# Kernel tuning notes

Measured on AMD Instinct MI355X. Metric: run time of the kernel, lower is better.

## Reference

```python
import jax, jax.numpy as jnp
import numpy as np

C, H, R, INTER = 1024, 16, 16, 2816  # hidden, heads, lora rank, mlp intermediate
B, N = 2, 2048
EPS = 1e-5


def setup_inputs() -> dict:
    key = jax.random.key(0)
    ks = iter(jax.random.split(key, 48))
    w = lambda shape: jax.random.normal(next(ks), shape, jnp.float32) * 0.02
    d = {}
    d["x"] = jax.random.normal(next(ks), (B, N, C), jnp.float32)
    d["y"] = jax.random.normal(next(ks), (B, N, C), jnp.float32)
    d["c"] = jax.random.normal(next(ks), (B, C), jnp.float32)
    # LayerNorms
    d["gx_w"] = jnp.ones((C,)); d["gx_b"] = jnp.zeros((C,))
    d["gy_w"] = jnp.ones((C,)); d["gy_b"] = jnp.zeros((C,))
    # adaLN: SiLU -> Linear(C, 6C)
    d["ada_w"] = w((C, 6 * C)); d["ada_b"] = jnp.zeros((6 * C,))
    # two DoRA cross-attentions
    for p in ("xy", "yx"):
        d[p + "_qkv"] = w((C, 3 * C))
        d[p + "_mag"] = jnp.ones((1, H, 1, 1))
        d[p + "_la"] = w((C, R))
        d[p + "_lb"] = w((R, C))
        d[p + "_proj"] = w((C, C))
    # two HGRN recurrent attentions
    for p in ("ax", "ay"):
        d[p + "_wi"] = w((C, C))
        d[p + "_wf"] = w((C, C))
        d[p + "_wg"] = w((C, C))
        d[p + "_wo"] = w((C, C))
        d[p + "_gn"] = jnp.ones((C,))
    # two gated MLPs
    for p in ("mx", "my"):
        d[p + "_gate"] = w((C, 2 * INTER))
        d[p + "_down"] = w((INTER, C))
    return d


def _ln(v, wgt, b):
    m = v.mean(-1, keepdims=True)
    var = ((v - m) ** 2).mean(-1, keepdims=True)
    return (v - m) / jnp.sqrt(var + EPS) * wgt + b


def _modulate(v, shift, scale):
    return v * (1.0 + scale[:, None, :]) + shift[:, None, :]


def _dora_attn(q_in, Wqkv, mag, la, lb, Wp):
    # NOTE: source ignores key/value args -> self-attention on query stream
    Bq, Nq, Cq = q_in.shape
    D = Cq // H
    qkv = (q_in @ Wqkv).reshape(Bq, Nq, 3, H, D).transpose(2, 0, 3, 1, 4)
    q, k, v = qkv[0], qkv[1], qkv[2]  # [B,H,N,D]
    delta = (q_in @ la) @ lb  # LoRA delta injected into Q
    q = q + mag * delta.reshape(Bq, Nq, H, D).transpose(0, 2, 1, 3)
    attn = jax.nn.softmax(jnp.einsum('bhnd,bhmd->bhnm', q, k) * (D ** -0.5), axis=-1)
    o = jnp.einsum('bhnm,bhmd->bhnd', attn, v).transpose(0, 2, 1, 3).reshape(Bq, Nq, Cq)
    return o @ Wp


def _hgrn_attn(v, wi, wf, wg, wo, gn):
    Bv, Nv, Cv = v.shape
    D = Cv // H
    f = jax.nn.sigmoid(v @ wf)
    i = jax.nn.silu(v @ wi) * (1.0 - f)
    def step(h, ft_it):
        ft, it = ft_it
        h = ft * h + it
        return h, h
    _, hs = jax.lax.scan(step, jnp.zeros((Bv, Cv), v.dtype),
                         (f.transpose(1, 0, 2), i.transpose(1, 0, 2)))
    h = hs.transpose(1, 0, 2).reshape(Bv, Nv, H, D)
    h = h / jnp.sqrt((h * h).mean(-1, keepdims=True) + EPS)  # per-head RMSNorm
    h = (h * gn.reshape(H, D)).reshape(Bv, Nv, Cv)
    return (h * jax.nn.silu(v @ wg)) @ wo


def _mlp(v, wgate, wdown):
    u = v @ wgate
    gate, val = jnp.split(u, 2, axis=-1)
    return (jax.nn.silu(gate) * val) @ wdown


def reference(x, y, c, gx_w, gx_b, gy_w, gy_b, ada_w, ada_b,
              xy_qkv, xy_mag, xy_la, xy_lb, xy_proj,
              yx_qkv, yx_mag, yx_la, yx_lb, yx_proj,
              ax_wi, ax_wf, ax_wg, ax_wo, ax_gn,
              ay_wi, ay_wf, ay_wg, ay_wo, ay_gn,
              mx_gate, mx_down, my_gate, my_down):
    mods = jax.nn.silu(c) @ ada_w + ada_b
    sh_msa, sc_msa, g_msa, sh_mlp, sc_mlp, g_mlp = jnp.split(mods, 6, axis=1)
    x_norm = _ln(x, gx_w, gx_b)
    y_norm = _ln(y, gy_w, gy_b)
    x = x + g_msa[:, None, :] * _dora_attn(x_norm, xy_qkv, xy_mag, xy_la, xy_lb, xy_proj)
    y = y + g_msa[:, None, :] * _dora_attn(y_norm, yx_qkv, yx_mag, yx_la, yx_lb, yx_proj)
    x = x + g_msa[:, None, :] * _hgrn_attn(_modulate(x_norm, sh_msa, sc_msa), ax_wi, ax_wf, ax_wg, ax_wo, ax_gn)
    y = y + g_msa[:, None, :] * _hgrn_attn(_modulate(y_norm, sh_msa, sc_msa), ay_wi, ay_wf, ay_wg, ay_wo, ay_gn)
    x = x + g_mlp[:, None, :] * _mlp(_modulate(_ln(x, gx_w, gx_b), sh_mlp, sc_mlp), mx_gate, mx_down)
    y = y + g_mlp[:, None, :] * _mlp(_modulate(_ln(y, gy_w, gy_b), sh_mlp, sc_mlp), my_gate, my_down)
    return (x, y)
```

## Files before the change

kernel.cpp:

```cpp
#include <hip/hip_runtime.h>
#include <stdint.h>

#define NTOK 2048
#define CDIM 1024
#define ROWS 4096
#define MODS_STRIDE 6144
#define INTERDIM 2816
#define NCHUNK 32
#define CHLEN (NTOK/NCHUNK)

typedef unsigned short u16;
typedef __bf16 bf16x8 __attribute__((ext_vector_type(8)));
typedef float f32x4 __attribute__((ext_vector_type(4)));
typedef float f32x16 __attribute__((ext_vector_type(16)));
typedef u16 u16x8 __attribute__((ext_vector_type(8)));
typedef unsigned int u32x4 __attribute__((ext_vector_type(4)));

__device__ __forceinline__ float b2f(u16 u){
  union { unsigned int i; float f; } v; v.i = ((unsigned int)u) << 16; return v.f;
}
__device__ __forceinline__ u16 f2b(float f){
  union { float f; unsigned int i; } v; v.f = f;
  unsigned int i = v.i;
  unsigned int r = i + 0x7FFFu + ((i >> 16) & 1u);
  return (u16)(r >> 16);
}
__device__ __forceinline__ float sigm(float x){ return 1.f/(1.f+__expf(-x)); }
__device__ __forceinline__ float wredsum(float v){
#pragma unroll
  for (int o=32;o>0;o>>=1) v += __shfl_xor(v,o);
  return v;
}
__device__ __forceinline__ void async16(const void* g, void* l){
  __builtin_amdgcn_global_load_lds(
      (const __attribute__((address_space(1))) unsigned int*)g,
      (__attribute__((address_space(3))) unsigned int*)l, 16, 0, 0);
}
__device__ __forceinline__ unsigned cvt_pk_bf16(float lo, float hi){
  unsigned r;
  asm("v_cvt_pk_bf16_f32 %0, %1, %2" : "=v"(r) : "v"(lo), "v"(hi));
  return r;
}
__device__ __forceinline__ void permlane32_swap(unsigned &a, unsigned &b){
  asm volatile("v_permlane32_swap_b32 %0, %1" : "+v"(a), "+v"(b));
}

__global__ __launch_bounds__(512) void gemm_bt(
    const u16* __restrict__ Ain, const u16* __restrict__ Bt,
    int M, int N, int K, int epi,
    u16* __restrict__ outB,
    float* __restrict__ dest, const float* __restrict__ gate)
{
  __shared__ u16 smem[2][2][2][8192];

  const int nwg  = gridDim.x * gridDim.y;
  const int orig = blockIdx.y * gridDim.x + blockIdx.x;
  const int qch  = nwg >> 3, rch = nwg & 7;
  const int xcd  = orig & 7, loc = orig >> 3;
  const int swzb = (xcd < rch ? xcd*(qch+1) : rch*(qch+1) + (xcd-rch)*qch) + loc;
  const int m0 = (swzb / gridDim.x) * 256;
  const int n0 = (swzb % gridDim.x) * 256;

  const int kchunk = K / gridDim.z;
  const int kbase  = blockIdx.z * kchunk;
  const int NT = kchunk >> 6;

  const int tid = threadIdx.x;
  const int w = tid >> 6, lane = tid & 63;
  const int quad = lane >> 4, l16 = lane & 15;
  const int wm = w >> 2, wn = w & 3;
  const int sx = (l16 & 7) << 4;

  int soff[2];
#pragma unroll
  for (int j=0;j<2;++j){
    const int row = (w*2 + j)*8 + (lane >> 3);
    soff[j] = row*(K*2) + (((lane & 7) ^ (row & 7)) << 4);
  }

  const char* pA0 = (const char*)(Ain + (size_t)m0*K       + kbase);
  const char* pA1 = (const char*)(Ain + (size_t)(m0+128)*K + kbase);
  const char* pB0 = (const char*)(Bt  + (size_t)n0*K       + kbase);
  const char* pB1 = (const char*)(Bt  + (size_t)(n0+128)*K + kbase);

  auto stage = [&](const char* base, int t, u16* region){
#pragma unroll
    for (int j=0;j<2;++j)
      async16(base + (size_t)t*128 + soff[j], (char*)region + (w*2+j)*1024);
  };

  f32x4 acc[8][4] = {};
  bf16x8 af[4][2];
  bf16x8 bq[4][2];

  stage(pA0, 0, &smem[0][0][0][0]);
  stage(pA1, 0, &smem[0][0][1][0]);
  stage(pB0, 0, &smem[0][1][0][0]);
  stage(pB1, 0, &smem[0][1][1][0]);
  if (NT > 1){
    stage(pA0, 1, &smem[1][0][0][0]);
    asm volatile("s_waitcnt vmcnt(2)" ::: "memory");
  } else {
    asm volatile("s_waitcnt vmcnt(0)" ::: "memory");
  }
  __builtin_amdgcn_s_barrier();

#pragma unroll 1
  for (int t=0; t<NT; ++t){
    const int s  = t & 1;
    const int s1 = s ^ 1;
    const char* Ah = (const char*)&smem[s][0][wm][0];
    const char* Bh = (const char*)&smem[s][1][wn>>1][0];
    const int bb = (wn & 1) * 64;

#pragma unroll
    for (int mf=0; mf<4; ++mf)
#pragma unroll
      for (int ks=0; ks<2; ++ks){
        const int b = ((mf*16 + l16)*128 + ks*64 + quad*16) ^ sx;
        af[mf][ks] = *reinterpret_cast<const bf16x8*>(Ah + b);
      }
#pragma unroll
    for (int nf=0; nf<2; ++nf)
#pragma unroll
      for (int ks=0; ks<2; ++ks){
        const int b = ((bb + nf*16 + l16)*128 + ks*64 + quad*16) ^ sx;
        bq[nf][ks] = *reinterpret_cast<const bf16x8*>(Bh + b);
      }
    if (t+1 < NT) stage(pA1, t+1, &smem[s1][0][1][0]);
    __builtin_amdgcn_sched_barrier(0);
    __builtin_amdgcn_s_barrier();
    asm volatile("s_waitcnt lgkmcnt(0)" ::: "memory");
    __builtin_amdgcn_sched_barrier(0);
    __builtin_amdgcn_s_setprio(1);
#pragma unroll
    for (int mf=0; mf<4; ++mf)
#pragma unroll
      for (int nf=0; nf<2; ++nf)
#pragma unroll
        for (int ks=0; ks<2; ++ks)
          acc[mf][nf] = __builtin_amdgcn_mfma_f32_16x16x32_bf16(af[mf][ks], bq[nf][ks], acc[mf][nf], 0,0,0);
    __builtin_amdgcn_s_setprio(0);
    __builtin_amdgcn_sched_barrier(0);
    __builtin_amdgcn_s_barrier();

#pragma unroll
    for (int nf=0; nf<2; ++nf)
#pragma unroll
      for (int ks=0; ks<2; ++ks){
        const int b = ((bb + (2+nf)*16 + l16)*128 + ks*64 + quad*16) ^ sx;
        bq[2+nf][ks] = *reinterpret_cast<const bf16x8*>(Bh + b);
      }
    if (t+1 < NT) stage(pB0, t+1, &smem[s1][1][0][0]);
    __builtin_amdgcn_sched_barrier(0);
    __builtin_amdgcn_s_barrier();
    asm volatile("s_waitcnt lgkmcnt(0)" ::: "memory");
    __builtin_amdgcn_sched_barrier(0);
    __builtin_amdgcn_s_setprio(1);
#pragma unroll
    for (int mf=0; mf<4; ++mf)
#pragma unroll
      for (int nf=0; nf<2; ++nf)
#pragma unroll
        for (int ks=0; ks<2; ++ks)
          acc[mf][2+nf] = __builtin_amdgcn_mfma_f32_16x16x32_bf16(af[mf][ks], bq[2+nf][ks], acc[mf][2+nf], 0,0,0);
    __builtin_amdgcn_s_setprio(0);
    __builtin_amdgcn_sched_barrier(0);
    __builtin_amdgcn_s_barrier();

#pragma unroll
    for (int mf=0; mf<4; ++mf)
#pragma unroll
      for (int ks=0; ks<2; ++ks){
        const int b = ((64 + mf*16 + l16)*128 + ks*64 + quad*16) ^ sx;
        af[mf][ks] = *reinterpret_cast<const bf16x8*>(Ah + b);
      }
    if (t+1 < NT) stage(pB1, t+1, &smem[s1][1][1][0]);
    __builtin_amdgcn_sched_barrier(0);
    __builtin_amdgcn_s_barrier();
    asm volatile("s_waitcnt lgkmcnt(0)" ::: "memory");
    __builtin_amdgcn_sched_barrier(0);
    __builtin_amdgcn_s_setprio(1);
#pragma unroll
    for (int mf=0; mf<4; ++mf)
#pragma unroll
      for (int nf=0; nf<2; ++nf)
#pragma unroll
        for (int ks=0; ks<2; ++ks)
          acc[4+mf][2+nf] = __builtin_amdgcn_mfma_f32_16x16x32_bf16(af[mf][ks], bq[2+nf][ks], acc[4+mf][2+nf], 0,0,0);
    __builtin_amdgcn_s_setprio(0);
    __builtin_amdgcn_sched_barrier(0);
    __builtin_amdgcn_s_barrier();

    if (t+2 < NT) stage(pA0, t+2, &smem[s][0][0][0]);
    __builtin_amdgcn_sched_barrier(0);
    __builtin_amdgcn_s_barrier();
    __builtin_amdgcn_s_setprio(1);
#pragma unroll
    for (int mf=0; mf<4; ++mf)
#pragma unroll
      for (int nf=0; nf<2; ++nf)
#pragma unroll
        for (int ks=0; ks<2; ++ks)
          acc[4+mf][nf] = __builtin_amdgcn_mfma_f32_16x16x32_bf16(af[mf][ks], bq[nf][ks], acc[4+mf][nf], 0,0,0);
    __builtin_amdgcn_s_setprio(0);
    __builtin_amdgcn_sched_barrier(0);
    if (t+2 < NT) asm volatile("s_waitcnt vmcnt(2)" ::: "memory");
    else          asm volatile("s_waitcnt vmcnt(0)" ::: "memory");
    __builtin_amdgcn_s_barrier();
  }

#pragma unroll
  for (int i=0;i<8;++i){
    const int row = m0 + wm*128 + (i>>2)*64 + (i&3)*16 + quad*4;
#pragma unroll
    for (int j=0;j<4;++j){
      const int col = n0 + wn*64 + j*16 + l16;
#pragma unroll
      for (int r=0;r<4;++r){
        const float v = acc[i][j][r];
        const size_t idx = (size_t)(row + r)*N + col;
        if (epi==1){ outB[idx] = f2b(v); }
        else {
          const int b = (row + r) >> 11;
          atomicAdd(&dest[idx], gate[b*MODS_STRIDE + col] * v);
        }
      }
    }
  }
}

struct TDesc { const float* src; u16* dst; int rows; int cols; int base; int dstride; int doff; };
struct TPack { TDesc d[16]; };

__global__ __launch_bounds__(256) void transpose_all(TPack p, int nmat)
{
  __shared__ float t[64][65];
  const int bid = blockIdx.x;
  int mi = 0;
#pragma unroll 1
  while (mi+1 < nmat && bid >= p.d[mi+1].base) ++mi;
  const TDesc D = p.d[mi];
  const int tid2   = bid - D.base;
  const int tilesx = D.cols >> 6;
  const int r0 = (tid2 / tilesx) * 64;
  const int c0 = (tid2 % tilesx) * 64;
  const int tx = threadIdx.x & 63, ty = threadIdx.x >> 6;
  for (int i=ty;i<64;i+=4)
    t[i][tx] = D.src[(size_t)(r0+i)*D.cols + c0 + tx];
  __syncthreads();
  const int wx = threadIdx.x & 31, wy = threadIdx.x >> 5;
  for (int c=wy;c<64;c+=8){
    const unsigned lo = f2b(t[2*wx  ][c]);
    const unsigned hi = f2b(t[2*wx+1][c]);
    *reinterpret_cast<unsigned*>(&D.dst[(size_t)(c0+c)*D.dstride + D.doff + r0 + 2*wx]) = lo | (hi<<16);
  }
}

__global__ __launch_bounds__(256) void lora_fold(
    const float* __restrict__ la, const float* __restrict__ lb,
    const float* __restrict__ mag, u16* __restrict__ WqkvT)
{
  const unsigned idx = blockIdx.x*256u + threadIdx.x;
  const int k = idx & 1023, n = idx >> 10;
  float s = 0.f;
#pragma unroll
  for (int r=0;r<16;++r)
    s = fmaf(la[k*16+r], lb[r*1024+n], s);
  const float m = mag[n>>6];
  const unsigned o = (unsigned)n*1024u + k;
  WqkvT[o] = f2b(b2f(WqkvT[o]) + m*s);
}

__global__ __launch_bounds__(256) void ln_kernel(
    const float* __restrict__ xin,
    const float* __restrict__ w, const float* __restrict__ bias,
    const float* __restrict__ mods, int sh_off, int sc_off,
    u16* __restrict__ out_norm, u16* __restrict__ out_mod,
    float* __restrict__ out_xw)
{
  const int row = blockIdx.x;
  const int b = row >> 11;
  const int t = threadIdx.x;
  float v[4];
#pragma unroll
  for (int e=0;e<4;++e)
    v[e] = xin[(size_t)row*CDIM + t*4+e];
  float s  = v[0]+v[1]+v[2]+v[3];
  float ss = v[0]*v[0]+v[1]*v[1]+v[2]*v[2]+v[3]*v[3];
  s = wredsum(s); ss = wredsum(ss);
  __shared__ float rs[4], rss[4];
  const int wv = t>>6;
  if ((t&63)==0){ rs[wv]=s; rss[wv]=ss; }
  __syncthreads();
  s  = rs[0]+rs[1]+rs[2]+rs[3];
  ss = rss[0]+rss[1]+rss[2]+rss[3];
  const float mean = s * (1.f/1024.f);
  const float var  = ss * (1.f/1024.f) - mean*mean;
  const float rinv = rsqrtf(var + 1e-5f);
#pragma unroll
  for (int e=0;e<4;++e){
    const int c = t*4+e;
    const float nv = (v[e]-mean)*rinv*w[c] + bias[c];
    if (out_norm) out_norm[(size_t)row*CDIM+c] = f2b(nv);
    if (out_mod){
      const float sc = mods[b*MODS_STRIDE + sc_off + c];
      const float sh = mods[b*MODS_STRIDE + sh_off + c];
      out_mod[(size_t)row*CDIM+c] = f2b(nv*(1.f+sc)+sh);
    }
    if (out_xw) out_xw[(size_t)row*CDIM+c] = v[e];
  }
}

__global__ __launch_bounds__(256) void ada_init(
    const float* __restrict__ ab, float* __restrict__ mods)
{
  const int j = blockIdx.x*256 + threadIdx.x;
  const int jj = (j >= MODS_STRIDE) ? j - MODS_STRIDE : j;
  mods[j] = ab[jj];
}

__global__ __launch_bounds__(256) void ada_split(
    const float* __restrict__ cin, const float* __restrict__ aw,
    float* __restrict__ mods)
{
  const int j  = blockIdx.x*256 + threadIdx.x;
  const int k0 = blockIdx.y*64;
  float s0 = 0.f, s1 = 0.f;
  for (int k=k0; k<k0+64; ++k){
    const float wv = aw[(size_t)k*MODS_STRIDE + j];
    const float c0 = cin[k], c1 = cin[CDIM + k];
    s0 = fmaf(c0*sigm(c0), wv, s0);
    s1 = fmaf(c1*sigm(c1), wv, s1);
  }
  atomicAdd(&mods[j], s0);
  atomicAdd(&mods[MODS_STRIDE + j], s1);
}

__global__ __launch_bounds__(256) void attn_mfma(
    const u16* __restrict__ qkv, u16* __restrict__ AH)
{
  __shared__ u16 Kl[64*64];
  __shared__ u16 Vt[64*64];
  const int t = threadIdx.x;
  const int w = t>>6, lane = t&63;
  const int l32 = lane & 31, hi = lane >> 5;
  const int qt = blockIdx.x, h = blockIdx.y, b = blockIdx.z;
  const size_t rowbase = (size_t)b*NTOK;

  bf16x8 qf[4];
  {
    const size_t gr = rowbase + qt*128 + w*32 + l32;
    const u16* qp = qkv + gr*3072 + h*64;
#pragma unroll
    for (int ds=0; ds<4; ++ds){
      const u16x8 qa = *reinterpret_cast<const u16x8*>(qp + ds*16 + hi*8);
#pragma unroll
      for (int j=0;j<8;++j)
        qf[ds][j] = (__bf16)(b2f(qa[j]) * 0.125f);
    }
  }

  const u16* ksrc[2]; int kwr[2];
#pragma unroll
  for (int it=0; it<2; ++it){
    const int e = it*256 + t;
    const int key = e>>3, ch = e&7;
    ksrc[it] = qkv + (rowbase + key)*3072 + 1024 + h*64 + ch*8;
    kwr[it]  = key*128 + ((ch ^ (key&7)) << 4);
  }
  const u16* vsrc[2]; int vwr[2][8];
#pragma unroll
  for (int it=0; it<2; ++it){
    const int d0 = (w*2 + it)*8;
    vsrc[it] = qkv + (rowbase + lane)*3072 + 2048 + h*64 + d0;
#pragma unroll
    for (int j=0;j<8;++j){
      const int d = d0 + j;
      vwr[it][j] = d*128 + (((lane>>3) ^ (d&7)) << 4) + (lane&7)*2;
    }
  }
  int kra[2][4];
#pragma unroll
  for (int st=0; st<2; ++st)
#pragma unroll
    for (int ds=0; ds<4; ++ds){
      const int key = st*32 + l32;
      kra[st][ds] = key*128 + (((ds*2 + hi) ^ (key&7)) << 4);
    }
  int vra[2][2][2];
#pragma unroll
  for (int st=0; st<2; ++st)
#pragma unroll
    for (int ks=0; ks<2; ++ks)
#pragma unroll
      for (int dt=0; dt<2; ++dt){
        const int d = dt*32 + l32;
        vra[st][ks][dt] = d*128 + (((st*4 + ks*2 + hi) ^ (d&7)) << 4);
      }

  const size_t KSTRIDE = (size_t)64*3072;

  u16x8 kA[2], vA[2], kB[2], vB[2];
#pragma unroll
  for (int it=0; it<2; ++it){
    kA[it] = *reinterpret_cast<const u16x8*>(ksrc[it]);
    vA[it] = *reinterpret_cast<const u16x8*>(vsrc[it]);
  }

  float l_part = 0.f;
  f32x16 oacc[2] = {};

  auto step = [&](u16x8 (&kk)[2], u16x8 (&vv)[2], int kbn,
                  u16x8 (&kn)[2], u16x8 (&vn)[2]){
#pragma unroll
    for (int it=0; it<2; ++it){
      *reinterpret_cast<u16x8*>((char*)Kl + kwr[it]) = kk[it];
#pragma unroll
      for (int j=0;j<8;++j)
        *reinterpret_cast<u16*>((char*)Vt + vwr[it][j]) = vv[it][j];
    }
    __syncthreads();
    {
      const size_t off = (size_t)kbn * KSTRIDE;
#pragma unroll
      for (int it=0; it<2; ++it){
        kn[it] = *reinterpret_cast<const u16x8*>(ksrc[it] + off);
        vn[it] = *reinterpret_cast<const u16x8*>(vsrc[it] + off);
      }
    }
    f32x16 sacc[2] = {};
#pragma unroll
    for (int st=0; st<2; ++st)
#pragma unroll
      for (int ds=0; ds<4; ++ds){
        const bf16x8 af = *reinterpret_cast<const bf16x8*>((char*)Kl + kra[st][ds]);
        sacc[st] = __builtin_amdgcn_mfma_f32_32x32x16_bf16(af, qf[ds], sacc[st], 0,0,0);
      }
#pragma unroll
    for (int st=0; st<2; ++st)
#pragma unroll
      for (int r=0;r<16;++r){
        const float pv = __expf(sacc[st][r]);
        sacc[st][r] = pv;
        l_part += pv;
      }
#pragma unroll
    for (int st=0; st<2; ++st){
      unsigned wd[8];
#pragma unroll
      for (int m=0;m<8;++m)
        wd[m] = cvt_pk_bf16(sacc[st][2*m], sacc[st][2*m+1]);
      permlane32_swap(wd[0], wd[2]);
      permlane32_swap(wd[1], wd[3]);
      permlane32_swap(wd[4], wd[6]);
      permlane32_swap(wd[5], wd[7]);
      u32x4 paw[2];
      paw[0] = u32x4{wd[0], wd[1], wd[2], wd[3]};
      paw[1] = u32x4{wd[4], wd[5], wd[6], wd[7]};
#pragma unroll
      for (int ks=0; ks<2; ++ks){
        const bf16x8 pa = *reinterpret_cast<const bf16x8*>(&paw[ks]);
#pragma unroll
        for (int dt=0; dt<2; ++dt){
          const bf16x8 vb = *reinterpret_cast<const bf16x8*>((char*)Vt + vra[st][ks][dt]);
          oacc[dt] = __builtin_amdgcn_mfma_f32_32x32x16_bf16(pa, vb, oacc[dt], 0,0,0);
        }
      }
    }
    __syncthreads();
  };

#pragma unroll 1
  for (int kb=0; kb<32; kb+=2){
    step(kA, vA, (kb+1 < 32 ? kb+1 : 31), kB, vB);
    step(kB, vB, (kb+2 < 32 ? kb+2 : 31), kA, vA);
  }

  const float l_run = l_part + __shfl_xor(l_part, 32);

#pragma unroll
  for (int r=0;r<16;++r){
    const int crow = (r&3) + 8*(r>>2) + 4*hi;
    const float li = __shfl(l_run, crow);
    const size_t grow = rowbase + qt*128 + w*32 + crow;
#pragma unroll
    for (int dt=0; dt<2; ++dt)
      AH[grow*2048 + h*64 + dt*32 + l32] = f2b(oacc[dt][r] / li);
  }
}

__global__ __launch_bounds__(256) void scan_p1(
    const u16* __restrict__ FIG, float* __restrict__ cA, float* __restrict__ cH)
{
  const unsigned int idx = blockIdx.x*256u + threadIdx.x;
  const unsigned int c = idx & 1023u, chunk = (idx>>10)&(NCHUNK-1), b = idx>>15;
  float A = 1.f, h = 0.f;
  const size_t base = ((size_t)b*NTOK + chunk*CHLEN) * 3072;
  for (int t=0;t<CHLEN;++t){
    const float F = b2f(FIG[base + (size_t)t*3072 + c]);
    const float I = b2f(FIG[base + (size_t)t*3072 + 1024 + c]);
    const float f = sigm(F);
    const float il = I*sigm(I) * (1.f - f);
    A *= f;
    h = fmaf(f, h, il);
  }
  cA[idx] = A; cH[idx] = h;
}

__global__ __launch_bounds__(256) void scan_p2(
    const float* __restrict__ cA, const float* __restrict__ cH, float* __restrict__ Hinit)
{
  const unsigned int idx = blockIdx.x*256u + threadIdx.x;
  const unsigned int b = idx>>10, c = idx&1023u;
  float h = 0.f;
#pragma unroll
  for (int ch=0;ch<NCHUNK;++ch){
    const unsigned int q = (b*NCHUNK + ch)*1024 + c;
    Hinit[q] = h;
    h = fmaf(cA[q], h, cH[q]);
  }
}

__global__ __launch_bounds__(256) void scan_p3(
    const u16* __restrict__ FIG, const float* __restrict__ Hinit, u16* __restrict__ Hb)
{
  const unsigned int idx = blockIdx.x*256u + threadIdx.x;
  const unsigned int c = idx & 1023u, chunk = (idx>>10)&(NCHUNK-1), b = idx>>15;
  float h = Hinit[idx];
  const size_t base = ((size_t)b*NTOK + chunk*CHLEN) * 3072;
  const size_t obase = ((size_t)b*NTOK + chunk*CHLEN) * CDIM;
  for (int t=0;t<CHLEN;++t){
    const float F = b2f(FIG[base + (size_t)t*3072 + c]);
    const float I = b2f(FIG[base + (size_t)t*3072 + 1024 + c]);
    const float f = sigm(F);
    const float il = I*sigm(I) * (1.f - f);
    h = fmaf(f, h, il);
    Hb[obase + (size_t)t*CDIM + c] = f2b(h);
  }
}

__global__ __launch_bounds__(256) void hgrn_post(
    const u16* __restrict__ Hb, const u16* __restrict__ FIG,
    const float* __restrict__ gn, u16* __restrict__ AH)
{
  const int row = blockIdx.x;
  const int t = threadIdx.x;
  float hv[4]; float ss = 0.f;
#pragma unroll
  for (int e=0;e<4;++e){
    hv[e] = b2f(Hb[(size_t)row*CDIM + t*4 + e]);
    ss = fmaf(hv[e], hv[e], ss);
  }
#pragma unroll
  for (int o=1;o<16;o<<=1) ss += __shfl_xor(ss, o);
  const float rinv = rsqrtf(ss*(1.f/64.f) + 1e-5f);
#pragma unroll
  for (int e=0;e<4;++e){
    const int c = t*4+e;
    const float g = b2f(FIG[(size_t)row*3072 + 2048 + c]);
    AH[(size_t)row*2048 + 1024 + c] = f2b(hv[e]*rinv*gn[c] * g*sigm(g));
  }
}

__global__ __launch_bounds__(256) void act_kernel(
    const u16* __restrict__ U, u16* __restrict__ A)
{
  const unsigned int i = blockIdx.x*256u + threadIdx.x;
  const unsigned int r = i / INTERDIM, j = i % INTERDIM;
  const float g = b2f(U[(size_t)r*(2*INTERDIM) + j]);
  const float v = b2f(U[(size_t)r*(2*INTERDIM) + INTERDIM + j]);
  A[i] = f2b(g*sigm(g)*v);
}

__global__ __launch_bounds__(256) void fill_fail(float* __restrict__ out)
{
  const unsigned int i = blockIdx.x*256u + threadIdx.x;
  out[i] = 1234.5f;
}

static void run_stream(hipStream_t stream,
    const float* Xin, const float* LNW, const float* LNB,
    const float* MAG, const float* LA, const float* LBw, const float* GN,
    float* mods, float* xw,
    u16* WqkvT, const u16* WpwT, const u16* WhgrnT,
    const u16* WgateT, const u16* WdownT,
    u16* x_norm, u16* v_h, u16* qkvb, u16* delta, u16* AH,
    float* cA, float* cH, float* Hinit, u16* U, u16* actb)
{
  u16* FIG    = qkvb;
  u16* Hb     = delta;
  u16* mlp_in = x_norm;

  lora_fold<<<4096,256,0,stream>>>(LA, LBw, MAG, WqkvT);

  ln_kernel<<<ROWS,256,0,stream>>>(Xin, LNW, LNB, mods, 0, 1024, x_norm, v_h, xw);

  gemm_bt<<<dim3(12,16),512,0,stream>>>(x_norm, WqkvT, ROWS,3072,1024, 1, qkvb, nullptr, nullptr);
  attn_mfma<<<dim3(16,16,2),256,0,stream>>>(qkvb, AH);

  gemm_bt<<<dim3(12,16),512,0,stream>>>(v_h, WhgrnT, ROWS,3072,1024, 1, FIG, nullptr, nullptr);
  scan_p1<<<2*NCHUNK*1024/256,256,0,stream>>>(FIG, cA, cH);
  scan_p2<<<8,256,0,stream>>>(cA, cH, Hinit);
  scan_p3<<<2*NCHUNK*1024/256,256,0,stream>>>(FIG, Hinit, Hb);
  hgrn_post<<<ROWS,256,0,stream>>>(Hb, FIG, GN, AH);

  gemm_bt<<<dim3(4,16,4),512,0,stream>>>(AH, WpwT, ROWS,1024,2048, 2, nullptr, xw, mods+2048);

  ln_kernel<<<ROWS,256,0,stream>>>(xw, LNW, LNB, mods, 3072, 4096, nullptr, mlp_in, nullptr);
  gemm_bt<<<dim3(22,16),512,0,stream>>>(mlp_in, WgateT, ROWS,5632,1024, 1, U, nullptr, nullptr);
  act_kernel<<<ROWS*INTERDIM/256,256,0,stream>>>(U, actb);
  gemm_bt<<<dim3(4,16,4),512,0,stream>>>(actb, WdownT, ROWS,1024,2816, 2, nullptr, xw, mods+5120);
}

extern "C" void kernel_launch(void* const* d_in, const int* in_sizes, int n_in,
                              void* d_out, int out_size, void* d_ws, size_t ws_size,
                              hipStream_t stream)
{
  const float* X    = (const float*)d_in[0];
  const float* Y    = (const float*)d_in[1];
  const float* Cc   = (const float*)d_in[2];
  const float* GXW  = (const float*)d_in[3];
  const float* GXB  = (const float*)d_in[4];
  const float* GYW  = (const float*)d_in[5];
  const float* GYB  = (const float*)d_in[6];
  const float* ADAW = (const float*)d_in[7];
  const float* ADAB = (const float*)d_in[8];
  const float* XY_QKV = (const float*)d_in[9];
  const float* XY_MAG = (const float*)d_in[10];
  const float* XY_LA  = (const float*)d_in[11];
  const float* XY_LB  = (const float*)d_in[12];
  const float* XY_PROJ= (const float*)d_in[13];
  const float* YX_QKV = (const float*)d_in[14];
  const float* YX_MAG = (const float*)d_in[15];
  const float* YX_LA  = (const float*)d_in[16];
  const float* YX_LB  = (const float*)d_in[17];
  const float* YX_PROJ= (const float*)d_in[18];
  const float* AX_WI = (const float*)d_in[19];
  const float* AX_WF = (const float*)d_in[20];
  const float* AX_WG = (const float*)d_in[21];
  const float* AX_WO = (const float*)d_in[22];
  const float* AX_GN = (const float*)d_in[23];
  const float* AY_WI = (const float*)d_in[24];
  const float* AY_WF = (const float*)d_in[25];
  const float* AY_WG = (const float*)d_in[26];
  const float* AY_WO = (const float*)d_in[27];
  const float* AY_GN = (const float*)d_in[28];
  const float* MX_GATE = (const float*)d_in[29];
  const float* MX_DOWN = (const float*)d_in[30];
  const float* MY_GATE = (const float*)d_in[31];
  const float* MY_DOWN = (const float*)d_in[32];
  float* OUT = (float*)d_out;

  char* p = (char*)d_ws;
  size_t off = 0;
  auto alloc = [&](size_t bytes)->char*{
    char* r = p + off;
    off = (off + bytes + 255) & ~(size_t)255;
    return r;
  };
  float* mods  = (float*)alloc(2*MODS_STRIDE*sizeof(float));
  u16* WqkvT0  = (u16*)alloc((size_t)3072*1024*2);
  u16* WqkvT1  = (u16*)alloc((size_t)3072*1024*2);
  u16* WpwT0   = (u16*)alloc((size_t)1024*2048*2);
  u16* WpwT1   = (u16*)alloc((size_t)1024*2048*2);
  u16* WhgrnT0 = (u16*)alloc((size_t)3072*1024*2);
  u16* WhgrnT1 = (u16*)alloc((size_t)3072*1024*2);
  u16* WgateT0 = (u16*)alloc((size_t)5632*1024*2);
  u16* WgateT1 = (u16*)alloc((size_t)5632*1024*2);
  u16* WdownT0 = (u16*)alloc((size_t)1024*2816*2);
  u16* WdownT1 = (u16*)alloc((size_t)1024*2816*2);
  u16* x_norm  = (u16*)alloc((size_t)ROWS*CDIM*2);
  u16* v_h     = (u16*)alloc((size_t)ROWS*CDIM*2);
  u16* qkvb    = (u16*)alloc((size_t)ROWS*3072*2);
  u16* delta   = (u16*)alloc((size_t)ROWS*CDIM*2);
  u16* AH      = (u16*)alloc((size_t)ROWS*2048*2);
  float* cA    = (float*)alloc((size_t)2*NCHUNK*1024*sizeof(float));
  float* cH    = (float*)alloc((size_t)2*NCHUNK*1024*sizeof(float));
  float* Hinit = (float*)alloc((size_t)2*NCHUNK*1024*sizeof(float));
  u16* U       = (u16*)alloc((size_t)ROWS*5632*2);
  u16* actb    = (u16*)alloc((size_t)ROWS*INTERDIM*2);

  if (off > ws_size){
    fill_fail<<<(2*ROWS*CDIM)/256,256,0,stream>>>(OUT);
    return;
  }

  ada_init<<<2*MODS_STRIDE/256,256,0,stream>>>(ADAB, mods);
  ada_split<<<dim3(MODS_STRIDE/256,16),256,0,stream>>>(Cc, ADAW, mods);

  TPack tp; int base = 0; int ndesc = 0;
  auto add = [&](const float* s, u16* d2, int rows, int cols, int dstride, int doff){
    tp.d[ndesc].src = s; tp.d[ndesc].dst = d2;
    tp.d[ndesc].rows = rows; tp.d[ndesc].cols = cols; tp.d[ndesc].base = base;
    tp.d[ndesc].dstride = dstride; tp.d[ndesc].doff = doff;
    base += (rows>>6)*(cols>>6); ++ndesc;
  };
  add(XY_QKV,  WqkvT0, 1024, 3072, 1024, 0);
  add(XY_PROJ, WpwT0,  1024, 1024, 2048, 0);
  add(AX_WO,   WpwT0,  1024, 1024, 2048, 1024);
  add(AX_WF, WhgrnT0,               1024, 1024, 1024, 0);
  add(AX_WI, WhgrnT0 + 1024*1024,   1024, 1024, 1024, 0);
  add(AX_WG, WhgrnT0 + 2*1024*1024, 1024, 1024, 1024, 0);
  add(MX_GATE, WgateT0, 1024, 5632, 1024, 0);
  add(MX_DOWN, WdownT0, 2816, 1024, 2816, 0);
  add(YX_QKV,  WqkvT1, 1024, 3072, 1024, 0);
  add(YX_PROJ, WpwT1,  1024, 1024, 2048, 0);
  add(AY_WO,   WpwT1,  1024, 1024, 2048, 1024);
  add(AY_WF, WhgrnT1,               1024, 1024, 1024, 0);
  add(AY_WI, WhgrnT1 + 1024*1024,   1024, 1024, 1024, 0);
  add(AY_WG, WhgrnT1 + 2*1024*1024, 1024, 1024, 1024, 0);
  add(MY_GATE, WgateT1, 1024, 5632, 1024, 0);
  add(MY_DOWN, WdownT1, 2816, 1024, 2816, 0);
  transpose_all<<<base,256,0,stream>>>(tp, ndesc);

  run_stream(stream, X, GXW, GXB, XY_MAG, XY_LA, XY_LB, AX_GN,
             mods, OUT,
             WqkvT0, WpwT0, WhgrnT0, WgateT0, WdownT0,
             x_norm, v_h, qkvb, delta, AH,
             cA, cH, Hinit, U, actb);

  run_stream(stream, Y, GYW, GYB, YX_MAG, YX_LA, YX_LB, AY_GN,
             mods, OUT + (size_t)ROWS*CDIM,
             WqkvT1, WpwT1, WhgrnT1, WgateT1, WdownT1,
             x_norm, v_h, qkvb, delta, AH,
             cA, cH, Hinit, U, actb);
}
```

Measured before the change: 1.175 ms.

## Batch the x and y streams into single launches per stage

Every stage kernel (lora_fold, LN, GEMMs, attention, scan, hgrn_post, act) now takes pointer pairs and picks its stream from the block index. Each stage runs for both streams in one launch with twice the grid, which halves the launch count and fills the GPU better on the smaller grids such as the split-K GEMMs and the scans. The cost is a separate workspace for each stream, roughly doubling intermediate memory. A sequential per-stream fallback is kept for when the workspace is too small.

```diff
diff --git a/kernel.cpp b/kernel.cpp
--- a/kernel.cpp
+++ b/kernel.cpp
@@ -46,12 +46,21 @@
 }
 
 __global__ __launch_bounds__(512) void gemm_bt(
-    const u16* __restrict__ Ain, const u16* __restrict__ Bt,
-    int M, int N, int K, int epi,
-    u16* __restrict__ outB,
-    float* __restrict__ dest, const float* __restrict__ gate)
+    const u16* __restrict__ A0, const u16* __restrict__ A1,
+    const u16* __restrict__ B0, const u16* __restrict__ B1,
+    int M, int N, int K, int zsplit, int epi,
+    u16* __restrict__ o0, u16* __restrict__ o1,
+    float* __restrict__ d0, float* __restrict__ d1,
+    const float* __restrict__ gate)
 {
   __shared__ u16 smem[2][2][2][8192];
+
+  const int zs = blockIdx.z / zsplit;
+  const int kz = blockIdx.z % zsplit;
+  const u16* Ain = zs ? A1 : A0;
+  const u16* Bt  = zs ? B1 : B0;
+  u16* outB  = zs ? o1 : o0;
+  float* dest = zs ? d1 : d0;
 
   const int nwg  = gridDim.x * gridDim.y;
   const int orig = blockIdx.y * gridDim.x + blockIdx.x;
@@ -61,8 +70,8 @@
   const int m0 = (swzb / gridDim.x) * 256;
   const int n0 = (swzb % gridDim.x) * 256;
 
-  const int kchunk = K / gridDim.z;
-  const int kbase  = blockIdx.z * kchunk;
+  const int kchunk = K / zsplit;
+  const int kbase  = kz * kchunk;
   const int NT = kchunk >> 6;
 
   const int tid = threadIdx.x;
@@ -258,29 +267,47 @@
 }
 
 __global__ __launch_bounds__(256) void lora_fold(
-    const float* __restrict__ la, const float* __restrict__ lb,
-    const float* __restrict__ mag, u16* __restrict__ WqkvT)
-{
-  const unsigned idx = blockIdx.x*256u + threadIdx.x;
+    const float* __restrict__ la0, const float* __restrict__ la1,
+    const float* __restrict__ lb0, const float* __restrict__ lb1,
+    const float* __restrict__ mg0, const float* __restrict__ mg1,
+    u16* __restrict__ W0, u16* __restrict__ W1)
+{
+  const unsigned g = blockIdx.x*256u + threadIdx.x;
+  const int s = g >> 20;
+  const unsigned idx = g & 1048575u;
+  const float* la = s ? la1 : la0;
+  const float* lb = s ? lb1 : lb0;
+  const float* mag = s ? mg1 : mg0;
+  u16* W = s ? W1 : W0;
   const int k = idx & 1023, n = idx >> 10;
-  float s = 0.f;
+  float sum = 0.f;
 #pragma unroll
   for (int r=0;r<16;++r)
-    s = fmaf(la[k*16+r], lb[r*1024+n], s);
+    sum = fmaf(la[k*16+r], lb[r*1024+n], sum);
   const float m = mag[n>>6];
   const unsigned o = (unsigned)n*1024u + k;
-  WqkvT[o] = f2b(b2f(WqkvT[o]) + m*s);
+  W[o] = f2b(b2f(W[o]) + m*sum);
 }
 
 __global__ __launch_bounds__(256) void ln_kernel(
-    const float* __restrict__ xin,
-    const float* __restrict__ w, const float* __restrict__ bias,
+    const float* __restrict__ x0, const float* __restrict__ x1,
+    const float* __restrict__ w0, const float* __restrict__ w1,
+    const float* __restrict__ bi0, const float* __restrict__ bi1,
     const float* __restrict__ mods, int sh_off, int sc_off,
-    u16* __restrict__ out_norm, u16* __restrict__ out_mod,
-    float* __restrict__ out_xw)
-{
-  const int row = blockIdx.x;
+    u16* __restrict__ on0, u16* __restrict__ on1,
+    u16* __restrict__ om0, u16* __restrict__ om1,
+    float* __restrict__ ox0, float* __restrict__ ox1)
+{
+  const int gr = blockIdx.x;
+  const int sid = gr >> 12;
+  const int row = gr & (ROWS-1);
   const int b = row >> 11;
+  const float* xin  = sid ? x1  : x0;
+  const float* w    = sid ? w1  : w0;
+  const float* bias = sid ? bi1 : bi0;
+  u16* out_norm = sid ? on1 : on0;
+  u16* out_mod  = sid ? om1 : om0;
+  float* out_xw = sid ? ox1 : ox0;
   const int t = threadIdx.x;
   float v[4];
 #pragma unroll
@@ -338,14 +365,19 @@
 }
 
 __global__ __launch_bounds__(256) void attn_mfma(
-    const u16* __restrict__ qkv, u16* __restrict__ AH)
+    const u16* __restrict__ q0, const u16* __restrict__ q1,
+    u16* __restrict__ A0, u16* __restrict__ A1)
 {
   __shared__ u16 Kl[64*64];
   __shared__ u16 Vt[64*64];
   const int t = threadIdx.x;
   const int w = t>>6, lane = t&63;
   const int l32 = lane & 31, hi = lane >> 5;
-  const int qt = blockIdx.x, h = blockIdx.y, b = blockIdx.z;
+  const int qt = blockIdx.x, h = blockIdx.y;
+  const int zb = blockIdx.z;
+  const int b = zb & 1, sid = zb >> 1;
+  const u16* qkv = sid ? q1 : q0;
+  u16* AH = sid ? A1 : A0;
   const size_t rowbase = (size_t)b*NTOK;
 
   bf16x8 qf[4];
@@ -491,10 +523,14 @@
 }
 
 __global__ __launch_bounds__(256) void scan_p1(
-    const u16* __restrict__ FIG, float* __restrict__ cA, float* __restrict__ cH)
-{
-  const unsigned int idx = blockIdx.x*256u + threadIdx.x;
-  const unsigned int c = idx & 1023u, chunk = (idx>>10)&(NCHUNK-1), b = idx>>15;
+    const u16* __restrict__ F0, const u16* __restrict__ F1,
+    float* __restrict__ cA, float* __restrict__ cH)
+{
+  const unsigned g = blockIdx.x*256u + threadIdx.x;
+  const int s = g >> 16;
+  const unsigned idx = g & 65535u;
+  const u16* FIG = s ? F1 : F0;
+  const unsigned c = idx & 1023u, chunk = (idx>>10)&(NCHUNK-1), b = idx>>15;
   float A = 1.f, h = 0.f;
   const size_t base = ((size_t)b*NTOK + chunk*CHLEN) * 3072;
   for (int t=0;t<CHLEN;++t){
@@ -505,29 +541,35 @@
     A *= f;
     h = fmaf(f, h, il);
   }
-  cA[idx] = A; cH[idx] = h;
+  cA[g] = A; cH[g] = h;
 }
 
 __global__ __launch_bounds__(256) void scan_p2(
     const float* __restrict__ cA, const float* __restrict__ cH, float* __restrict__ Hinit)
 {
   const unsigned int idx = blockIdx.x*256u + threadIdx.x;
-  const unsigned int b = idx>>10, c = idx&1023u;
+  const unsigned int sb = idx>>10, c = idx&1023u;
   float h = 0.f;
 #pragma unroll
   for (int ch=0;ch<NCHUNK;++ch){
-    const unsigned int q = (b*NCHUNK + ch)*1024 + c;
+    const unsigned int q = (sb*NCHUNK + ch)*1024 + c;
     Hinit[q] = h;
     h = fmaf(cA[q], h, cH[q]);
   }
 }
 
 __global__ __launch_bounds__(256) void scan_p3(
-    const u16* __restrict__ FIG, const float* __restrict__ Hinit, u16* __restrict__ Hb)
-{
-  const unsigned int idx = blockIdx.x*256u + threadIdx.x;
-  const unsigned int c = idx & 1023u, chunk = (idx>>10)&(NCHUNK-1), b = idx>>15;
-  float h = Hinit[idx];
+    const u16* __restrict__ F0, const u16* __restrict__ F1,
+    const float* __restrict__ Hinit,
+    u16* __restrict__ H0, u16* __restrict__ H1)
+{
+  const unsigned g = blockIdx.x*256u + threadIdx.x;
+  const int s = g >> 16;
+  const unsigned idx = g & 65535u;
+  const u16* FIG = s ? F1 : F0;
+  u16* Hb = s ? H1 : H0;
+  const unsigned c = idx & 1023u, chunk = (idx>>10)&(NCHUNK-1), b = idx>>15;
+  float h = Hinit[g];
   const size_t base = ((size_t)b*NTOK + chunk*CHLEN) * 3072;
   const size_t obase = ((size_t)b*NTOK + chunk*CHLEN) * CDIM;
   for (int t=0;t<CHLEN;++t){
@@ -541,10 +583,18 @@
 }
 
 __global__ __launch_bounds__(256) void hgrn_post(
-    const u16* __restrict__ Hb, const u16* __restrict__ FIG,
-    const float* __restrict__ gn, u16* __restrict__ AH)
-{
-  const int row = blockIdx.x;
+    const u16* __restrict__ H0, const u16* __restrict__ H1,
+    const u16* __restrict__ F0, const u16* __restrict__ F1,
+    const float* __restrict__ g0, const float* __restrict__ g1,
+    u16* __restrict__ A0, u16* __restrict__ A1)
+{
+  const int gr = blockIdx.x;
+  const int s = gr >> 12;
+  const int row = gr & (ROWS-1);
+  const u16* Hb = s ? H1 : H0;
+  const u16* FIG = s ? F1 : F0;
+  const float* gn = s ? g1 : g0;
+  u16* AH = s ? A1 : A0;
   const int t = threadIdx.x;
   float hv[4]; float ss = 0.f;
 #pragma unroll
@@ -564,53 +614,25 @@
 }
 
 __global__ __launch_bounds__(256) void act_kernel(
-    const u16* __restrict__ U, u16* __restrict__ A)
-{
-  const unsigned int i = blockIdx.x*256u + threadIdx.x;
-  const unsigned int r = i / INTERDIM, j = i % INTERDIM;
-  const float g = b2f(U[(size_t)r*(2*INTERDIM) + j]);
+    const u16* __restrict__ U0, const u16* __restrict__ U1,
+    u16* __restrict__ A0, u16* __restrict__ A1)
+{
+  const unsigned g = blockIdx.x*256u + threadIdx.x;
+  const unsigned tot = (unsigned)ROWS*INTERDIM;
+  const int s = g >= tot;
+  const unsigned i = s ? g - tot : g;
+  const u16* U = s ? U1 : U0;
+  u16* A = s ? A1 : A0;
+  const unsigned r = i / INTERDIM, j = i % INTERDIM;
+  const float gg = b2f(U[(size_t)r*(2*INTERDIM) + j]);
   const float v = b2f(U[(size_t)r*(2*INTERDIM) + INTERDIM + j]);
-  A[i] = f2b(g*sigm(g)*v);
+  A[i] = f2b(gg*sigm(gg)*v);
 }
 
 __global__ __launch_bounds__(256) void fill_fail(float* __restrict__ out)
 {
   const unsigned int i = blockIdx.x*256u + threadIdx.x;
   out[i] = 1234.5f;
-}
-
-static void run_stream(hipStream_t stream,
-    const float* Xin, const float* LNW, const float* LNB,
-    const float* MAG, const float* LA, const float* LBw, const float* GN,
-    float* mods, float* xw,
-    u16* WqkvT, const u16* WpwT, const u16* WhgrnT,
-    const u16* WgateT, const u16* WdownT,
-    u16* x_norm, u16* v_h, u16* qkvb, u16* delta, u16* AH,
-    float* cA, float* cH, float* Hinit, u16* U, u16* actb)
-{
-  u16* FIG    = qkvb;
-  u16* Hb     = delta;
-  u16* mlp_in = x_norm;
-
-  lora_fold<<<4096,256,0,stream>>>(LA, LBw, MAG, WqkvT);
-
-  ln_kernel<<<ROWS,256,0,stream>>>(Xin, LNW, LNB, mods, 0, 1024, x_norm, v_h, xw);
-
-  gemm_bt<<<dim3(12,16),512,0,stream>>>(x_norm, WqkvT, ROWS,3072,1024, 1, qkvb, nullptr, nullptr);
-  attn_mfma<<<dim3(16,16,2),256,0,stream>>>(qkvb, AH);
-
-  gemm_bt<<<dim3(12,16),512,0,stream>>>(v_h, WhgrnT, ROWS,3072,1024, 1, FIG, nullptr, nullptr);
-  scan_p1<<<2*NCHUNK*1024/256,256,0,stream>>>(FIG, cA, cH);
-  scan_p2<<<8,256,0,stream>>>(cA, cH, Hinit);
-  scan_p3<<<2*NCHUNK*1024/256,256,0,stream>>>(FIG, Hinit, Hb);
-  hgrn_post<<<ROWS,256,0,stream>>>(Hb, FIG, GN, AH);
-
-  gemm_bt<<<dim3(4,16,4),512,0,stream>>>(AH, WpwT, ROWS,1024,2048, 2, nullptr, xw, mods+2048);
-
-  ln_kernel<<<ROWS,256,0,stream>>>(xw, LNW, LNB, mods, 3072, 4096, nullptr, mlp_in, nullptr);
-  gemm_bt<<<dim3(22,16),512,0,stream>>>(mlp_in, WgateT, ROWS,5632,1024, 1, U, nullptr, nullptr);
-  act_kernel<<<ROWS*INTERDIM/256,256,0,stream>>>(U, actb);
-  gemm_bt<<<dim3(4,16,4),512,0,stream>>>(actb, WdownT, ROWS,1024,2816, 2, nullptr, xw, mods+5120);
 }
 
 extern "C" void kernel_launch(void* const* d_in, const int* in_sizes, int n_in,
@@ -651,6 +673,8 @@
   const float* MY_GATE = (const float*)d_in[31];
   const float* MY_DOWN = (const float*)d_in[32];
   float* OUT = (float*)d_out;
+  float* xw0 = OUT;
+  float* xw1 = OUT + (size_t)ROWS*CDIM;
 
   char* p = (char*)d_ws;
   size_t off = 0;
@@ -659,6 +683,7 @@
     off = (off + bytes + 255) & ~(size_t)255;
     return r;
   };
+
   float* mods  = (float*)alloc(2*MODS_STRIDE*sizeof(float));
   u16* WqkvT0  = (u16*)alloc((size_t)3072*1024*2);
   u16* WqkvT1  = (u16*)alloc((size_t)3072*1024*2);
@@ -670,20 +695,39 @@
   u16* WgateT1 = (u16*)alloc((size_t)5632*1024*2);
   u16* WdownT0 = (u16*)alloc((size_t)1024*2816*2);
   u16* WdownT1 = (u16*)alloc((size_t)1024*2816*2);
-  u16* x_norm  = (u16*)alloc((size_t)ROWS*CDIM*2);
-  u16* v_h     = (u16*)alloc((size_t)ROWS*CDIM*2);
-  u16* qkvb    = (u16*)alloc((size_t)ROWS*3072*2);
-  u16* delta   = (u16*)alloc((size_t)ROWS*CDIM*2);
-  u16* AH      = (u16*)alloc((size_t)ROWS*2048*2);
-  float* cA    = (float*)alloc((size_t)2*NCHUNK*1024*sizeof(float));
-  float* cH    = (float*)alloc((size_t)2*NCHUNK*1024*sizeof(float));
-  float* Hinit = (float*)alloc((size_t)2*NCHUNK*1024*sizeof(float));
-  u16* U       = (u16*)alloc((size_t)ROWS*5632*2);
-  u16* actb    = (u16*)alloc((size_t)ROWS*INTERDIM*2);
-
-  if (off > ws_size){
-    fill_fail<<<(2*ROWS*CDIM)/256,256,0,stream>>>(OUT);
-    return;
+
+  const size_t off_w = off;
+  u16* xn[2];  xn[0]  = (u16*)alloc((size_t)ROWS*CDIM*2);  xn[1]  = (u16*)alloc((size_t)ROWS*CDIM*2);
+  u16* vh[2];  vh[0]  = (u16*)alloc((size_t)ROWS*CDIM*2);  vh[1]  = (u16*)alloc((size_t)ROWS*CDIM*2);
+  u16* qb[2];  qb[0]  = (u16*)alloc((size_t)ROWS*3072*2);  qb[1]  = (u16*)alloc((size_t)ROWS*3072*2);
+  u16* Hb[2];  Hb[0]  = (u16*)alloc((size_t)ROWS*CDIM*2);  Hb[1]  = (u16*)alloc((size_t)ROWS*CDIM*2);
+  u16* AH[2];  AH[0]  = (u16*)alloc((size_t)ROWS*2048*2);  AH[1]  = (u16*)alloc((size_t)ROWS*2048*2);
+  u16* Ub[2];  Ub[0]  = (u16*)alloc((size_t)ROWS*5632*2);  Ub[1]  = (u16*)alloc((size_t)ROWS*5632*2);
+  u16* ab[2];  ab[0]  = (u16*)alloc((size_t)ROWS*INTERDIM*2); ab[1] = (u16*)alloc((size_t)ROWS*INTERDIM*2);
+  float* cA    = (float*)alloc((size_t)4*NCHUNK*1024*sizeof(float));
+  float* cH    = (float*)alloc((size_t)4*NCHUNK*1024*sizeof(float));
+  float* Hinit = (float*)alloc((size_t)4*NCHUNK*1024*sizeof(float));
+  const bool batched = (off <= ws_size);
+
+  if (!batched){
+    off = off_w;
+    u16* x_norm  = (u16*)alloc((size_t)ROWS*CDIM*2);
+    u16* v_h     = (u16*)alloc((size_t)ROWS*CDIM*2);
+    u16* qkvb    = (u16*)alloc((size_t)ROWS*3072*2);
+    u16* hb      = (u16*)alloc((size_t)ROWS*CDIM*2);
+    u16* ah      = (u16*)alloc((size_t)ROWS*2048*2);
+    float* scA   = (float*)alloc((size_t)2*NCHUNK*1024*sizeof(float));
+    float* scH   = (float*)alloc((size_t)2*NCHUNK*1024*sizeof(float));
+    float* sHin  = (float*)alloc((size_t)2*NCHUNK*1024*sizeof(float));
+    u16* Uu      = (u16*)alloc((size_t)ROWS*5632*2);
+    u16* acts    = (u16*)alloc((size_t)ROWS*INTERDIM*2);
+    if (off > ws_size){
+      fill_fail<<<(2*ROWS*CDIM)/256,256,0,stream>>>(OUT);
+      return;
+    }
+    xn[0]=xn[1]=x_norm; vh[0]=vh[1]=v_h; qb[0]=qb[1]=qkvb; Hb[0]=Hb[1]=hb;
+    AH[0]=AH[1]=ah; Ub[0]=Ub[1]=Uu; ab[0]=ab[1]=acts;
+    cA=scA; cH=scH; Hinit=sHin;
   }
 
   ada_init<<<2*MODS_STRIDE/256,256,0,stream>>>(ADAB, mods);
@@ -714,15 +758,64 @@
   add(MY_DOWN, WdownT1, 2816, 1024, 2816, 0);
   transpose_all<<<base,256,0,stream>>>(tp, ndesc);
 
-  run_stream(stream, X, GXW, GXB, XY_MAG, XY_LA, XY_LB, AX_GN,
-             mods, OUT,
-             WqkvT0, WpwT0, WhgrnT0, WgateT0, WdownT0,
-             x_norm, v_h, qkvb, delta, AH,
-             cA, cH, Hinit, U, actb);
-
-  run_stream(stream, Y, GYW, GYB, YX_MAG, YX_LA, YX_LB, AY_GN,
-             mods, OUT + (size_t)ROWS*CDIM,
-             WqkvT1, WpwT1, WhgrnT1, WgateT1, WdownT1,
-             x_norm, v_h, qkvb, delta, AH,
-             cA, cH, Hinit, U, actb);
-}
+  if (batched){
+    lora_fold<<<8192,256,0,stream>>>(XY_LA, YX_LA, XY_LB, YX_LB, XY_MAG, YX_MAG, WqkvT0, WqkvT1);
+    ln_kernel<<<2*ROWS,256,0,stream>>>(X, Y, GXW, GYW, GXB, GYB, mods, 0, 1024,
+                                       xn[0], xn[1], vh[0], vh[1], xw0, xw1);
+    gemm_bt<<<dim3(12,16,2),512,0,stream>>>(xn[0], xn[1], WqkvT0, WqkvT1,
+        ROWS,3072,1024, 1,1, qb[0], qb[1], nullptr,nullptr, nullptr);
+    attn_mfma<<<dim3(16,16,4),256,0,stream>>>(qb[0], qb[1], AH[0], AH[1]);
+    gemm_bt<<<dim3(12,16,2),512,0,stream>>>(vh[0], vh[1], WhgrnT0, WhgrnT1,
+        ROWS,3072,1024, 1,1, qb[0], qb[1], nullptr,nullptr, nullptr);
+    scan_p1<<<512,256,0,stream>>>(qb[0], qb[1], cA, cH);
+    scan_p2<<<16,256,0,stream>>>(cA, cH, Hinit);
+    scan_p3<<<512,256,0,stream>>>(qb[0], qb[1], Hinit, Hb[0], Hb[1]);
+    hgrn_post<<<2*ROWS,256,0,stream>>>(Hb[0], Hb[1], qb[0], qb[1], AX_GN, AY_GN, AH[0], AH[1]);
+    gemm_bt<<<dim3(4,16,8),512,0,stream>>>(AH[0], AH[1], WpwT0, WpwT1,
+        ROWS,1024,2048, 4,2, nullptr,nullptr, xw0, xw1, mods+2048);
+    ln_kernel<<<2*ROWS,256,0,stream>>>(xw0, xw1, GXW, GYW, GXB, GYB, mods, 3072, 4096,
+                                       nullptr,nullptr, xn[0], xn[1], nullptr,nullptr);
+    gemm_bt<<<dim3(22,16,2),512,0,stream>>>(xn[0], xn[1], WgateT0, WgateT1,
+        ROWS,5632,1024, 1,1, Ub[0], Ub[1], nullptr,nullptr, nullptr);
+    act_kernel<<<2*ROWS*INTERDIM/256,256,0,stream>>>(Ub[0], Ub[1], ab[0], ab[1]);
+    gemm_bt<<<dim3(4,16,8),512,0,stream>>>(ab[0], ab[1], WdownT0, WdownT1,
+        ROWS,1024,2816, 4,2, nullptr,nullptr, xw0, xw1, mods+5120);
+  } else {
+    const float* Xs[2]   = {X, Y};
+    const float* LNWs[2] = {GXW, GYW};
+    const float* LNBs[2] = {GXB, GYB};
+    const float* MAGs[2] = {XY_MAG, YX_MAG};
+    const float* LAs[2]  = {XY_LA, YX_LA};
+    const float* LBs[2]  = {XY_LB, YX_LB};
+    const float* GNs[2]  = {AX_GN, AY_GN};
+    u16* Wq[2] = {WqkvT0, WqkvT1};
+    u16* Wp[2] = {WpwT0, WpwT1};
+    u16* Wh[2] = {WhgrnT0, WhgrnT1};
+    u16* Wg[2] = {WgateT0, WgateT1};
+    u16* Wd[2] = {WdownT0, WdownT1};
+    float* xws[2] = {xw0, xw1};
+    for (int s=0; s<2; ++s){
+      lora_fold<<<4096,256,0,stream>>>(LAs[s], LAs[s], LBs[s], LBs[s], MAGs[s], MAGs[s], Wq[s], Wq[s]);
+      ln_kernel<<<ROWS,256,0,stream>>>(Xs[s], Xs[s], LNWs[s], LNWs[s], LNBs[s], LNBs[s],
+          mods, 0, 1024, xn[0], xn[0], vh[0], vh[0], xws[s], xws[s]);
+      gemm_bt<<<dim3(12,16,1),512,0,stream>>>(xn[0], xn[0], Wq[s], Wq[s],
+          ROWS,3072,1024, 1,1, qb[0], qb[0], nullptr,nullptr, nullptr);
+      attn_mfma<<<dim3(16,16,2),256,0,stream>>>(qb[0], qb[0], AH[0], AH[0]);
+      gemm_bt<<<dim3(12,16,1),512,0,stream>>>(vh[0], vh[0], Wh[s], Wh[s],
+          ROWS,3072,1024, 1,1, qb[0], qb[0], nullptr,nullptr, nullptr);
+      scan_p1<<<256,256,0,stream>>>(qb[0], qb[0], cA, cH);
+      scan_p2<<<8,256,0,stream>>>(cA, cH, Hinit);
+      scan_p3<<<256,256,0,stream>>>(qb[0], qb[0], Hinit, Hb[0], Hb[0]);
+      hgrn_post<<<ROWS,256,0,stream>>>(Hb[0], Hb[0], qb[0], qb[0], GNs[s], GNs[s], AH[0], AH[0]);
+      gemm_bt<<<dim3(4,16,4),512,0,stream>>>(AH[0], AH[0], Wp[s], Wp[s],
+          ROWS,1024,2048, 4,2, nullptr,nullptr, xws[s], xws[s], mods+2048);
+      ln_kernel<<<ROWS,256,0,stream>>>(xws[s], xws[s], LNWs[s], LNWs[s], LNBs[s], LNBs[s],
+          mods, 3072, 4096, nullptr,nullptr, xn[0], xn[0], nullptr,nullptr);
+      gemm_bt<<<dim3(22,16,1),512,0,stream>>>(xn[0], xn[0], Wg[s], Wg[s],
+          ROWS,5632,1024, 1,1, Ub[0], Ub[0], nullptr,nullptr, nullptr);
+      act_kernel<<<ROWS*INTERDIM/256,256,0,stream>>>(Ub[0], Ub[0], ab[0], ab[0]);
+      gemm_bt<<<dim3(4,16,4),512,0,stream>>>(ab[0], ab[0], Wd[s], Wd[s],
+          ROWS,1024,2816, 4,2, nullptr,nullptr, xws[s], xws[s], mods+5120);
+    }
+  }
+}
```

Result: no change. 1.192 ms (+1.4%).
